# Kernel tuning notes

Hardware: AMD Instinct MI355X
Metric: run time of the kernel (lower is better)

Reference implementation:

```python
import jax, jax.numpy as jnp
import numpy as np

G = 16        # groups / heads
DG = 128      # per-group dim (2048/16)
F = 2048      # feat dim (representation_size)
N = 2048      # num_rois
M = 2048      # num_nongt_rois


def setup_inputs() -> dict:
    key = jax.random.key(0)
    ks = jax.random.split(key, 8)
    std = np.float32(0.02)
    return {
        "roi_feat": jax.random.normal(ks[0], (N, F), jnp.float32),
        "ref_feat": jax.random.normal(ks[1], (M, F), jnp.float32),
        "Wq_w": jax.random.normal(ks[2], (F, F), jnp.float32) * std,
        "Wq_b": jnp.zeros((F,), jnp.float32),
        "Wk_w": jax.random.normal(ks[3], (F, F), jnp.float32) * std,
        "Wk_b": jnp.zeros((F,), jnp.float32),
        # grouped 1x1 conv weight [2048, 2048, 1, 1] squeezed to [F, F];
        # group g maps input channels [g*F_g_in] -> output channels [g*DG:(g+1)*DG]
        "Wv_w": jax.random.normal(ks[4], (F, F), jnp.float32) * np.float32(0.01),
        "Wv_b": jnp.zeros((F,), jnp.float32),
    }


def reference(roi_feat, ref_feat, Wq_w, Wq_b, Wk_w, Wk_b, Wv_w, Wv_b):
    n = roi_feat.shape[0]
    scale = np.float32(1.0 / np.sqrt(DG))
    # torch Linear: y = x @ W.T + b
    q = (roi_feat @ Wq_w.T + Wq_b).reshape(n, G, DG)      # [N, G, DG]
    k = (ref_feat @ Wk_w.T + Wk_b).reshape(-1, G, DG)     # [M, G, DG]
    aff = jnp.einsum("ngd,mgd->ngm", q, k) * scale        # [N, G, M]
    attn = jax.nn.softmax(aff, axis=-1)
    # weighted values: v is raw ref_feat, per original
    ov = jnp.einsum("ngm,mf->ngf", attn, ref_feat)        # [N, G, F]
    # grouped 1x1 conv: per-group linear F -> DG
    Wv3 = Wv_w.reshape(G, DG, F)                          # [G, DG, F]
    out = jnp.einsum("ngf,gdf->ngd", ov, Wv3) + Wv_b.reshape(G, DG)
    return out.reshape(n, G * DG)                          # [N, F]
```

## Files before the change

### kernel.cpp

```cpp
#include <hip/hip_runtime.h>
#include <hip/hip_bf16.h>

#define G_   16
#define DG_  128
#define F_   2048
#define N_   2048
#define M_   2048

typedef __attribute__((ext_vector_type(8))) short s16x8;
typedef __attribute__((ext_vector_type(4))) float f32x4;
typedef __attribute__((ext_vector_type(2))) unsigned int u32x2;

typedef const __attribute__((address_space(1))) void GV;
typedef __attribute__((address_space(3))) void LV;

__device__ inline unsigned short f2bf(float f) {
  unsigned u = __float_as_uint(f);
  u += 0x7fffu + ((u >> 16) & 1u);
  return (unsigned short)(u >> 16);
}

struct Cvt5Args { const float* s[5]; unsigned short* d[5]; };

__global__ __launch_bounds__(256)
void cvt5(Cvt5Args a) {
  unsigned u = blockIdx.x * 256 + threadIdx.x;
  if (u >= 5u * 524288u) return;
  int seg = u >> 19;
  unsigned off = u & 524287u;
  const float4* sp = (const float4*)(a.s[seg] + (size_t)off * 8);
  float4 x = sp[0], y = sp[1];
  uint4 o;
  o.x = (unsigned)f2bf(x.x) | ((unsigned)f2bf(x.y) << 16);
  o.y = (unsigned)f2bf(x.z) | ((unsigned)f2bf(x.w) << 16);
  o.z = (unsigned)f2bf(y.x) | ((unsigned)f2bf(y.y) << 16);
  o.w = (unsigned)f2bf(y.z) | ((unsigned)f2bf(y.w) << 16);
  *(uint4*)(a.d[seg] + (size_t)off * 8) = o;
}

struct GemmJobs {
  const unsigned short* A[3];
  const unsigned short* B[3];
  const float* bias[3];
  unsigned short* C[3];
  float osc[3];
};

__global__ __launch_bounds__(512, 2)
void gemm8(GemmJobs jb) {
  __shared__ __align__(16) char lds[131072];
  const int wg = (blockIdx.x & 7) * 24 + (blockIdx.x >> 3);
  const int j  = wg >> 6;
  const int bs = wg & 63;
  const unsigned short* A = jb.A[j];
  const unsigned short* B = jb.B[j];
  const float* bias = jb.bias[j];
  unsigned short* C = jb.C[j];
  const float osc = jb.osc[j];

  const int tid = threadIdx.x, lane = tid & 63, wv = tid >> 6;
  const int wm = wv >> 2, wn = wv & 3;
  const int l15 = lane & 15, l4 = lane >> 4;
  const int m0 = (bs >> 3) * 256, n0 = (bs & 7) * 256;
  const int slot = (l4 ^ ((l15 >> 1) & 3)) * 16;
  const int scol = (((lane & 3) ^ ((lane >> 3) & 3)) * 8);
  const int srow = wv * 16 + (lane >> 2);
  const int rA = wm * 128 + l15;
  const int rB = (wn >> 1) * 128 + (wn & 1) * 64 + l15;

  f32x4 acc[8][4];
#pragma unroll
  for (int i = 0; i < 8; ++i)
#pragma unroll
    for (int nf = 0; nf < 4; ++nf) acc[i][nf] = (f32x4){0.f, 0.f, 0.f, 0.f};

  auto stage = [&](int buf2, const unsigned short* Mat, int lbase, int h,
                   int row0, int k0) {
#pragma unroll
    for (int rb = 0; rb < 2; ++rb) {
      __builtin_amdgcn_global_load_lds(
          (GV*)(Mat + (size_t)(row0 + rb * 128 + srow) * F_ + k0 + h * 32 + scol),
          (LV*)(lds + buf2 * 65536 + lbase + h * 16384 + rb * 8192 + wv * 1024),
          16, 0, 0);
    }
  };

  stage(0, A, 0,     0, m0, 0);
  stage(0, B, 32768, 0, n0, 0);
  stage(0, A, 0,     1, m0, 0);
  stage(0, B, 32768, 1, n0, 0);
  asm volatile("s_waitcnt vmcnt(4)" ::: "memory");
  __builtin_amdgcn_sched_barrier(0);
  __builtin_amdgcn_s_barrier();

  const int NT = F_ / 64;
  for (int t = 0; t < NT; ++t) {
    const int buf = t & 1;
    const char* Lb = lds + buf * 65536;
    const bool pf = (t + 1 < NT);
    const int k1 = (t + 1) * 64;
    s16x8 af[4], bf[4];

    auto ldA = [&](int mf, int h) {
      return *(const s16x8*)(Lb + h * 16384 + (rA + mf * 16) * 64 + slot);
    };
    auto ldB = [&](int nf, int h) {
      return *(const s16x8*)(Lb + 32768 + h * 16384 + (rB + nf * 16) * 64 + slot);
    };

#pragma unroll
    for (int nf = 0; nf < 4; ++nf) bf[nf] = ldB(nf, 0);
#pragma unroll
    for (int i = 0; i < 4; ++i) af[i] = ldA(i, 0);
    if (pf) stage(buf ^ 1, A, 0, 0, m0, k1);
    __builtin_amdgcn_sched_barrier(0);
    __builtin_amdgcn_s_barrier();
    asm volatile("s_waitcnt lgkmcnt(0)" ::: "memory");
    __builtin_amdgcn_sched_barrier(0);
    __builtin_amdgcn_s_setprio(1);
#pragma unroll
    for (int i = 0; i < 4; ++i)
#pragma unroll
      for (int nf = 0; nf < 4; ++nf)
        acc[i][nf] = __builtin_amdgcn_mfma_f32_16x16x32_bf16(af[i], bf[nf], acc[i][nf], 0, 0, 0);
    __builtin_amdgcn_s_setprio(0);
    __builtin_amdgcn_sched_barrier(0);
    __builtin_amdgcn_s_barrier();

#pragma unroll
    for (int i = 0; i < 4; ++i) af[i] = ldA(4 + i, 0);
    if (pf) stage(buf ^ 1, B, 32768, 0, n0, k1);
    __builtin_amdgcn_sched_barrier(0);
    __builtin_amdgcn_s_barrier();
    asm volatile("s_waitcnt lgkmcnt(0)" ::: "memory");
    __builtin_amdgcn_sched_barrier(0);
    __builtin_amdgcn_s_setprio(1);
#pragma unroll
    for (int i = 0; i < 4; ++i)
#pragma unroll
      for (int nf = 0; nf < 4; ++nf)
        acc[4 + i][nf] = __builtin_amdgcn_mfma_f32_16x16x32_bf16(af[i], bf[nf], acc[4 + i][nf], 0, 0, 0);
    __builtin_amdgcn_s_setprio(0);
    if (pf) { asm volatile("s_waitcnt vmcnt(4)" ::: "memory"); }
    else    { asm volatile("s_waitcnt vmcnt(0)" ::: "memory"); }
    __builtin_amdgcn_sched_barrier(0);
    __builtin_amdgcn_s_barrier();

#pragma unroll
    for (int nf = 0; nf < 4; ++nf) bf[nf] = ldB(nf, 1);
#pragma unroll
    for (int i = 0; i < 4; ++i) af[i] = ldA(i, 1);
    if (pf) stage(buf ^ 1, A, 0, 1, m0, k1);
    __builtin_amdgcn_sched_barrier(0);
    __builtin_amdgcn_s_barrier();
    asm volatile("s_waitcnt lgkmcnt(0)" ::: "memory");
    __builtin_amdgcn_sched_barrier(0);
    __builtin_amdgcn_s_setprio(1);
#pragma unroll
    for (int i = 0; i < 4; ++i)
#pragma unroll
      for (int nf = 0; nf < 4; ++nf)
        acc[i][nf] = __builtin_amdgcn_mfma_f32_16x16x32_bf16(af[i], bf[nf], acc[i][nf], 0, 0, 0);
    __builtin_amdgcn_s_setprio(0);
    __builtin_amdgcn_sched_barrier(0);
    __builtin_amdgcn_s_barrier();

#pragma unroll
    for (int i = 0; i < 4; ++i) af[i] = ldA(4 + i, 1);
    if (pf) stage(buf ^ 1, B, 32768, 1, n0, k1);
    __builtin_amdgcn_sched_barrier(0);
    __builtin_amdgcn_s_barrier();
    asm volatile("s_waitcnt lgkmcnt(0)" ::: "memory");
    __builtin_amdgcn_sched_barrier(0);
    __builtin_amdgcn_s_setprio(1);
#pragma unroll
    for (int i = 0; i < 4; ++i)
#pragma unroll
      for (int nf = 0; nf < 4; ++nf)
        acc[4 + i][nf] = __builtin_amdgcn_mfma_f32_16x16x32_bf16(af[i], bf[nf], acc[4 + i][nf], 0, 0, 0);
    __builtin_amdgcn_s_setprio(0);
    if (pf) { asm volatile("s_waitcnt vmcnt(4)" ::: "memory"); }
    __builtin_amdgcn_sched_barrier(0);
    __builtin_amdgcn_s_barrier();
  }

#pragma unroll
  for (int nf = 0; nf < 4; ++nf) {
    int c = n0 + wn * 64 + nf * 16 + l15;
    float bv = bias ? bias[c] : 0.f;
#pragma unroll
    for (int mf = 0; mf < 8; ++mf) {
#pragma unroll
      for (int jj = 0; jj < 4; ++jj) {
        int r = m0 + wm * 128 + mf * 16 + l4 * 4 + jj;
        C[(size_t)r * F_ + c] = f2bf((acc[mf][nf][jj] + bv) * osc);
      }
    }
  }
}

__global__ __launch_bounds__(256, 2)
void attn_mfma(const unsigned short* __restrict__ Q,
               const unsigned short* __restrict__ K,
               const unsigned short* __restrict__ Vt,
               const float* __restrict__ vb,
               float* __restrict__ out) {
  __shared__ unsigned short Kt[2][64 * 128];
  __shared__ unsigned short Vts[2][128 * 64];
  __shared__ unsigned short Pt[4][16 * 64];
  const int tid = threadIdx.x, lane = tid & 63, wv = tid >> 6;
  const int l15 = lane & 15, l4 = lane >> 4;
  const int g = blockIdx.y;
  const int q0 = blockIdx.x * 64 + wv * 16;

  s16x8 qa[4];
#pragma unroll
  for (int kc = 0; kc < 4; ++kc)
    qa[kc] = *(const s16x8*)(Q + (size_t)(q0 + l15) * F_ + g * DG_ + kc * 32 + l4 * 8);

  f32x4 oa[8];
#pragma unroll
  for (int df = 0; df < 8; ++df) oa[df] = (f32x4){0.f, 0.f, 0.f, 0.f};
  float m_r = -1e30f, l_r = 0.f;

  const int ksw0 = (((lane & 15) ^ (lane >> 4)) * 8);
  const int ksw1 = (((lane & 15) ^ 4 ^ (lane >> 4)) * 8);
  const int vsw  = (((lane & 7) ^ (lane >> 3)) * 8);
  const int xorb = (l15 & 7) << 4;
  int csw[4];
#pragma unroll
  for (int kc = 0; kc < 4; ++kc) csw[kc] = (kc * 64 + l4 * 16) ^ xorb;

  auto stage = [&](int buf, int kv0) {
#pragma unroll
    for (int i = 0; i < 4; ++i) {
      int r0 = wv * 16 + i * 4;
      __builtin_amdgcn_global_load_lds(
          (GV*)(K + (size_t)(kv0 + r0 + (lane >> 4)) * F_ + g * DG_ + ((i & 1) ? ksw1 : ksw0)),
          (LV*)(&Kt[buf][r0 * 128]), 16, 0, 0);
    }
#pragma unroll
    for (int i = 0; i < 4; ++i) {
      int r0 = wv * 32 + i * 8;
      __builtin_amdgcn_global_load_lds(
          (GV*)(Vt + (size_t)(g * DG_ + r0 + (lane >> 3)) * M_ + kv0 + vsw),
          (LV*)(&Vts[buf][r0 * 64]), 16, 0, 0);
    }
  };

  stage(0, 0);
  __syncthreads();
  int cur = 0;
  unsigned short* Pw = &Pt[wv][0];

  for (int t = 0; t < M_ / 64; ++t) {
    if (t + 1 < M_ / 64) stage(cur ^ 1, (t + 1) * 64);
    const unsigned short* Kb = &Kt[cur][0];
    const unsigned short* Vb = &Vts[cur][0];

    f32x4 sf[4];
    __builtin_amdgcn_s_setprio(1);
#pragma unroll
    for (int kvf = 0; kvf < 4; ++kvf) {
      f32x4 s = (f32x4){0.f, 0.f, 0.f, 0.f};
#pragma unroll
      for (int kc = 0; kc < 4; ++kc) {
        s16x8 kf = *(const s16x8*)((const char*)Kb + (kvf * 16 + l15) * 256 + csw[kc]);
        s = __builtin_amdgcn_mfma_f32_16x16x32_bf16(kf, qa[kc], s, 0, 0, 0);
      }
      sf[kvf] = s;
    }
    __builtin_amdgcn_s_setprio(0);

    float tmax = sf[0][0];
#pragma unroll
    for (int kvf = 0; kvf < 4; ++kvf) {
      tmax = fmaxf(tmax, fmaxf(fmaxf(sf[kvf][0], sf[kvf][1]),
                               fmaxf(sf[kvf][2], sf[kvf][3])));
    }
    tmax = fmaxf(tmax, __shfl_xor(tmax, 16));
    tmax = fmaxf(tmax, __shfl_xor(tmax, 32));
    if (!__all(tmax <= m_r + 8.0f)) {
      float mnew = fmaxf(m_r, tmax);
      float corr = __builtin_amdgcn_exp2f(m_r - mnew);
      m_r = mnew;
      l_r *= corr;
      float c0 = __shfl(corr, l4 * 4 + 0);
      float c1 = __shfl(corr, l4 * 4 + 1);
      float c2 = __shfl(corr, l4 * 4 + 2);
      float c3 = __shfl(corr, l4 * 4 + 3);
#pragma unroll
      for (int df = 0; df < 8; ++df) {
        oa[df][0] *= c0; oa[df][1] *= c1; oa[df][2] *= c2; oa[df][3] *= c3;
      }
    }

    float psum = 0.f;
#pragma unroll
    for (int kvf = 0; kvf < 4; ++kvf) {
      float p0 = __builtin_amdgcn_exp2f(sf[kvf][0] - m_r);
      float p1 = __builtin_amdgcn_exp2f(sf[kvf][1] - m_r);
      float p2 = __builtin_amdgcn_exp2f(sf[kvf][2] - m_r);
      float p3 = __builtin_amdgcn_exp2f(sf[kvf][3] - m_r);
      psum += (p0 + p1) + (p2 + p3);
      u32x2 w;
      asm("v_cvt_pk_bf16_f32 %0, %1, %2" : "=v"(w.x) : "v"(p0), "v"(p1));
      asm("v_cvt_pk_bf16_f32 %0, %1, %2" : "=v"(w.y) : "v"(p2), "v"(p3));
      *(u32x2*)((char*)Pw + l15 * 128 + ((kvf * 32 + l4 * 8) ^ xorb)) = w;
    }
    psum += __shfl_xor(psum, 16);
    psum += __shfl_xor(psum, 32);
    l_r += psum;

    s16x8 pa0 = *(const s16x8*)((const char*)Pw + l15 * 128 + csw[0]);
    s16x8 pa1 = *(const s16x8*)((const char*)Pw + l15 * 128 + csw[1]);
    __builtin_amdgcn_s_setprio(1);
#pragma unroll
    for (int df = 0; df < 8; ++df) {
      s16x8 v0 = *(const s16x8*)((const char*)Vb + (df * 16 + l15) * 128 + csw[0]);
      s16x8 v1 = *(const s16x8*)((const char*)Vb + (df * 16 + l15) * 128 + csw[1]);
      oa[df] = __builtin_amdgcn_mfma_f32_16x16x32_bf16(pa0, v0, oa[df], 0, 0, 0);
      oa[df] = __builtin_amdgcn_mfma_f32_16x16x32_bf16(pa1, v1, oa[df], 0, 0, 0);
    }
    __builtin_amdgcn_s_setprio(0);
    __syncthreads();
    cur ^= 1;
  }

  float linv = 1.0f / l_r;
  float i0 = __shfl(linv, l4 * 4 + 0);
  float i1 = __shfl(linv, l4 * 4 + 1);
  float i2 = __shfl(linv, l4 * 4 + 2);
  float i3 = __shfl(linv, l4 * 4 + 3);
#pragma unroll
  for (int df = 0; df < 8; ++df) {
    int c = g * DG_ + df * 16 + l15;
    float bv = vb[c];
    out[(size_t)(q0 + l4 * 4 + 0) * F_ + c] = oa[df][0] * i0 + bv;
    out[(size_t)(q0 + l4 * 4 + 1) * F_ + c] = oa[df][1] * i1 + bv;
    out[(size_t)(q0 + l4 * 4 + 2) * F_ + c] = oa[df][2] * i2 + bv;
    out[(size_t)(q0 + l4 * 4 + 3) * F_ + c] = oa[df][3] * i3 + bv;
  }
}

extern "C" void kernel_launch(void* const* d_in, const int* in_sizes, int n_in,
                              void* d_out, int out_size, void* d_ws, size_t ws_size,
                              hipStream_t stream) {
  const float* roi  = (const float*)d_in[0];
  const float* ref  = (const float*)d_in[1];
  const float* Wq_w = (const float*)d_in[2];
  const float* Wq_b = (const float*)d_in[3];
  const float* Wk_w = (const float*)d_in[4];
  const float* Wk_b = (const float*)d_in[5];
  const float* Wv_w = (const float*)d_in[6];
  const float* Wv_b = (const float*)d_in[7];
  float* out = (float*)d_out;
  const size_t SEG = 4194304;
  const float cscale = 0.12751664508246770f;

  if (ws_size < 64ull * 1024 * 1024) return;
  unsigned short* roi_bf = (unsigned short*)d_ws;
  unsigned short* ref_bf = roi_bf + SEG;
  unsigned short* Wq_bf  = ref_bf + SEG;
  unsigned short* Wk_bf  = Wq_bf + SEG;
  unsigned short* Wv_bf  = Wk_bf + SEG;
  unsigned short* Qb     = Wv_bf + SEG;
  unsigned short* Kb     = Qb + SEG;
  unsigned short* Vtb    = Kb + SEG;

  Cvt5Args ca;
  ca.s[0] = roi;  ca.d[0] = roi_bf;
  ca.s[1] = ref;  ca.d[1] = ref_bf;
  ca.s[2] = Wq_w; ca.d[2] = Wq_bf;
  ca.s[3] = Wk_w; ca.d[3] = Wk_bf;
  ca.s[4] = Wv_w; ca.d[4] = Wv_bf;
  cvt5<<<10240, 256, 0, stream>>>(ca);

  GemmJobs jb;
  jb.A[0] = roi_bf; jb.B[0] = Wq_bf;  jb.bias[0] = Wq_b;    jb.C[0] = Qb;  jb.osc[0] = cscale;
  jb.A[1] = ref_bf; jb.B[1] = Wk_bf;  jb.bias[1] = Wk_b;    jb.C[1] = Kb;  jb.osc[1] = 1.0f;
  jb.A[2] = Wv_bf;  jb.B[2] = ref_bf; jb.bias[2] = nullptr; jb.C[2] = Vtb; jb.osc[2] = 1.0f;
  gemm8<<<192, 512, 0, stream>>>(jb);

  attn_mfma<<<dim3(N_ / 64, G_), 256, 0, stream>>>(Qb, Kb, Vtb, Wv_b, out);
}
```

Before: 142.1 us.

## Merge GEMM k-loop into two phases with combined A/B staging

Restructures the bf16 projection GEMM main loop from four half-tile phases per k-step into two phases. Each phase now loads all eight A fragments and issues A and B global-to-LDS prefetches together, then runs 32 MFMAs. This halves the number of barriers and waitcnt points per iteration, at the cost of more live fragment registers and fewer points where loads can overlap compute. The vmcnt(4) counts now refer to the combined A+B staging, which still matches four loads per staged half.

Result: no change. 143.1 us (+0.7%).

```diff
diff --git a/kernel.cpp b/kernel.cpp
--- a/kernel.cpp
+++ b/kernel.cpp
@@ -74,21 +74,22 @@
 #pragma unroll
     for (int nf = 0; nf < 4; ++nf) acc[i][nf] = (f32x4){0.f, 0.f, 0.f, 0.f};
 
-  auto stage = [&](int buf2, const unsigned short* Mat, int lbase, int h,
-                   int row0, int k0) {
+  auto stage_kh = [&](int buf2, int h, int k0) {
 #pragma unroll
     for (int rb = 0; rb < 2; ++rb) {
       __builtin_amdgcn_global_load_lds(
-          (GV*)(Mat + (size_t)(row0 + rb * 128 + srow) * F_ + k0 + h * 32 + scol),
-          (LV*)(lds + buf2 * 65536 + lbase + h * 16384 + rb * 8192 + wv * 1024),
+          (GV*)(A + (size_t)(m0 + rb * 128 + srow) * F_ + k0 + h * 32 + scol),
+          (LV*)(lds + buf2 * 65536 + h * 16384 + rb * 8192 + wv * 1024),
           16, 0, 0);
+      __builtin_amdgcn_global_load_lds(
+          (GV*)(B + (size_t)(n0 + rb * 128 + srow) * F_ + k0 + h * 32 + scol),
+          (LV*)(lds + buf2 * 65536 + 32768 + h * 16384 + rb * 8192 + wv * 1024),
+          16, 0, 0);
     }
   };
 
-  stage(0, A, 0,     0, m0, 0);
-  stage(0, B, 32768, 0, n0, 0);
-  stage(0, A, 0,     1, m0, 0);
-  stage(0, B, 32768, 1, n0, 0);
+  stage_kh(0, 0, 0);
+  stage_kh(0, 1, 0);
   asm volatile("s_waitcnt vmcnt(4)" ::: "memory");
   __builtin_amdgcn_sched_barrier(0);
   __builtin_amdgcn_s_barrier();
@@ -99,7 +100,7 @@
     const char* Lb = lds + buf * 65536;
     const bool pf = (t + 1 < NT);
     const int k1 = (t + 1) * 64;
-    s16x8 af[4], bf[4];
+    s16x8 af[8], bf[4];
 
     auto ldA = [&](int mf, int h) {
       return *(const s16x8*)(Lb + h * 16384 + (rA + mf * 16) * 64 + slot);
@@ -111,74 +112,43 @@
 #pragma unroll
     for (int nf = 0; nf < 4; ++nf) bf[nf] = ldB(nf, 0);
 #pragma unroll
-    for (int i = 0; i < 4; ++i) af[i] = ldA(i, 0);
-    if (pf) stage(buf ^ 1, A, 0, 0, m0, k1);
+    for (int i = 0; i < 8; ++i) af[i] = ldA(i, 0);
+    if (pf) stage_kh(buf ^ 1, 0, k1);
     __builtin_amdgcn_sched_barrier(0);
     __builtin_amdgcn_s_barrier();
     asm volatile("s_waitcnt lgkmcnt(0)" ::: "memory");
     __builtin_amdgcn_sched_barrier(0);
     __builtin_amdgcn_s_setprio(1);
 #pragma unroll
-    for (int i = 0; i < 4; ++i)
+    for (int i = 0; i < 8; ++i)
 #pragma unroll
       for (int nf = 0; nf < 4; ++nf)
         acc[i][nf] = __builtin_amdgcn_mfma_f32_16x16x32_bf16(af[i], bf[nf], acc[i][nf], 0, 0, 0);
     __builtin_amdgcn_s_setprio(0);
     __builtin_amdgcn_sched_barrier(0);
+
+    if (pf) { asm volatile("s_waitcnt vmcnt(4)" ::: "memory"); }
+    else    { asm volatile("s_waitcnt vmcnt(0)" ::: "memory"); }
+    __builtin_amdgcn_sched_barrier(0);
     __builtin_amdgcn_s_barrier();
-
-#pragma unroll
-    for (int i = 0; i < 4; ++i) af[i] = ldA(4 + i, 0);
-    if (pf) stage(buf ^ 1, B, 32768, 0, n0, k1);
+#pragma unroll
+    for (int nf = 0; nf < 4; ++nf) bf[nf] = ldB(nf, 1);
+#pragma unroll
+    for (int i = 0; i < 8; ++i) af[i] = ldA(i, 1);
+    if (pf) stage_kh(buf ^ 1, 1, k1);
     __builtin_amdgcn_sched_barrier(0);
     __builtin_amdgcn_s_barrier();
     asm volatile("s_waitcnt lgkmcnt(0)" ::: "memory");
     __builtin_amdgcn_sched_barrier(0);
     __builtin_amdgcn_s_setprio(1);
 #pragma unroll
-    for (int i = 0; i < 4; ++i)
-#pragma unroll
-      for (int nf = 0; nf < 4; ++nf)
-        acc[4 + i][nf] = __builtin_amdgcn_mfma_f32_16x16x32_bf16(af[i], bf[nf], acc[4 + i][nf], 0, 0, 0);
-    __builtin_amdgcn_s_setprio(0);
-    if (pf) { asm volatile("s_waitcnt vmcnt(4)" ::: "memory"); }
-    else    { asm volatile("s_waitcnt vmcnt(0)" ::: "memory"); }
-    __builtin_amdgcn_sched_barrier(0);
-    __builtin_amdgcn_s_barrier();
-
-#pragma unroll
-    for (int nf = 0; nf < 4; ++nf) bf[nf] = ldB(nf, 1);
-#pragma unroll
-    for (int i = 0; i < 4; ++i) af[i] = ldA(i, 1);
-    if (pf) stage(buf ^ 1, A, 0, 1, m0, k1);
-    __builtin_amdgcn_sched_barrier(0);
-    __builtin_amdgcn_s_barrier();
-    asm volatile("s_waitcnt lgkmcnt(0)" ::: "memory");
-    __builtin_amdgcn_sched_barrier(0);
-    __builtin_amdgcn_s_setprio(1);
-#pragma unroll
-    for (int i = 0; i < 4; ++i)
+    for (int i = 0; i < 8; ++i)
 #pragma unroll
       for (int nf = 0; nf < 4; ++nf)
         acc[i][nf] = __builtin_amdgcn_mfma_f32_16x16x32_bf16(af[i], bf[nf], acc[i][nf], 0, 0, 0);
     __builtin_amdgcn_s_setprio(0);
     __builtin_amdgcn_sched_barrier(0);
-    __builtin_amdgcn_s_barrier();
-
-#pragma unroll
-    for (int i = 0; i < 4; ++i) af[i] = ldA(4 + i, 1);
-    if (pf) stage(buf ^ 1, B, 32768, 1, n0, k1);
-    __builtin_amdgcn_sched_barrier(0);
-    __builtin_amdgcn_s_barrier();
-    asm volatile("s_waitcnt lgkmcnt(0)" ::: "memory");
-    __builtin_amdgcn_sched_barrier(0);
-    __builtin_amdgcn_s_setprio(1);
-#pragma unroll
-    for (int i = 0; i < 4; ++i)
-#pragma unroll
-      for (int nf = 0; nf < 4; ++nf)
-        acc[4 + i][nf] = __builtin_amdgcn_mfma_f32_16x16x32_bf16(af[i], bf[nf], acc[4 + i][nf], 0, 0, 0);
-    __builtin_amdgcn_s_setprio(0);
+
     if (pf) { asm volatile("s_waitcnt vmcnt(4)" ::: "memory"); }
     __builtin_amdgcn_sched_barrier(0);
     __builtin_amdgcn_s_barrier();
```
